# Kernel tuning notes

Hardware: AMD Instinct MI355X
Metric: run time of the kernel (lower is better)

## Reference

```python
import jax, jax.numpy as jnp
import numpy as np

K = 8

def setup_inputs() -> dict:
    key = jax.random.key(0)
    x = jax.random.normal(key, (64, 256, 56, 56), dtype=jnp.float32)
    return {"x": x}

def reference(x) -> jnp.ndarray:
    b, c, h, w = x.shape
    hw = h * w
    k = K if K < hw else hw - 1
    # topk indices computed on detached data (stop_gradient)
    data = jax.lax.stop_gradient(x).reshape(-1, hw)  # [b*c, hw]
    _, indices = jax.lax.top_k(data, k)              # [b*c, k]
    rows = jnp.arange(data.shape[0])[:, None]
    weight = jnp.zeros_like(data).at[rows, indices].set(1.0)
    # masked spatial sum -> [b, c]
    y = (x * weight.reshape(b, c, h, w)).sum(axis=(-1, -2))
    return y
```

## Files before the change

kernel.cpp:

```cpp
#include <hip/hip_runtime.h>


#define CE(a, b) { float _hi = fmaxf((a), (b)); float _lo = fminf((a), (b)); (a) = _hi; (b) = _lo; }

#define SORT4(s0, s1, s2, s3) { CE(s0, s2); CE(s1, s3); CE(s0, s1); CE(s2, s3); CE(s1, s2); }

#define MERGE4(l0, l1, l2, l3, l4, l5, l6, l7, s0, s1, s2, s3) { \
    l4 = fmaxf(l4, s3); l5 = fmaxf(l5, s2); l6 = fmaxf(l6, s1); l7 = fmaxf(l7, s0); \
    CE(l0, l4); CE(l1, l5); CE(l2, l6); CE(l3, l7); \
    CE(l0, l2); CE(l1, l3); CE(l4, l6); CE(l5, l7); \
    CE(l0, l1); CE(l2, l3); CE(l4, l5); CE(l6, l7); }

#define RESORT8(m0, m1, m2, m3, m4, m5, m6, m7) { \
    CE(m0, m4); CE(m1, m5); CE(m2, m6); CE(m3, m7); \
    CE(m0, m2); CE(m1, m3); CE(m4, m6); CE(m5, m7); \
    CE(m0, m1); CE(m2, m3); CE(m4, m5); CE(m6, m7); }

__global__ __launch_bounds__(256) void topk8_sum_kernel(
    const float* __restrict__ x, float* __restrict__ out, int rows) {
    const int gw = (int)((blockIdx.x * blockDim.x + threadIdx.x) >> 6);
    const int lane = (int)(threadIdx.x & 63);
    if (gw >= rows) return;

    const float* __restrict__ row = x + (size_t)gw * 3136;

    float a0 = -INFINITY, a1 = -INFINITY, a2 = -INFINITY, a3 = -INFINITY,
          a4 = -INFINITY, a5 = -INFINITY, a6 = -INFINITY, a7 = -INFINITY;
    float b0 = -INFINITY, b1 = -INFINITY, b2 = -INFINITY, b3 = -INFINITY,
          b4 = -INFINITY, b5 = -INFINITY, b6 = -INFINITY, b7 = -INFINITY;

    #pragma unroll
    for (int it = 0; it < 6; ++it) {
        float4 u = *reinterpret_cast<const float4*>(row + (2 * it) * 256 + lane * 4);
        float4 v = *reinterpret_cast<const float4*>(row + (2 * it + 1) * 256 + lane * 4);
        float u0 = u.x, u1 = u.y, u2 = u.z, u3 = u.w;
        float v0 = v.x, v1 = v.y, v2 = v.z, v3 = v.w;
        SORT4(u0, u1, u2, u3);
        SORT4(v0, v1, v2, v3);
        MERGE4(a0, a1, a2, a3, a4, a5, a6, a7, u0, u1, u2, u3);
        MERGE4(b0, b1, b2, b3, b4, b5, b6, b7, v0, v1, v2, v3);
    }

    {
        float t = row[3072 + lane];
        CE(b0, t); CE(b1, t); CE(b2, t); CE(b3, t);
        CE(b4, t); CE(b5, t); CE(b6, t); CE(b7, t);
    }

    float r0 = fmaxf(a0, b7), r1 = fmaxf(a1, b6), r2 = fmaxf(a2, b5), r3 = fmaxf(a3, b4),
          r4 = fmaxf(a4, b3), r5 = fmaxf(a5, b2), r6 = fmaxf(a6, b1), r7 = fmaxf(a7, b0);
    RESORT8(r0, r1, r2, r3, r4, r5, r6, r7);

    #pragma unroll
    for (int m = 1; m <= 16; m <<= 1) {
        float c0 = __shfl_xor(r0, m, 64);
        float c1 = __shfl_xor(r1, m, 64);
        float c2 = __shfl_xor(r2, m, 64);
        float c3 = __shfl_xor(r3, m, 64);
        float c4 = __shfl_xor(r4, m, 64);
        float c5 = __shfl_xor(r5, m, 64);
        float c6 = __shfl_xor(r6, m, 64);
        float c7 = __shfl_xor(r7, m, 64);
        float m0 = fmaxf(r0, c7), m1 = fmaxf(r1, c6), m2 = fmaxf(r2, c5), m3 = fmaxf(r3, c4),
              m4 = fmaxf(r4, c3), m5 = fmaxf(r5, c2), m6 = fmaxf(r6, c1), m7 = fmaxf(r7, c0);
        RESORT8(m0, m1, m2, m3, m4, m5, m6, m7);
        r0 = m0; r1 = m1; r2 = m2; r3 = m3;
        r4 = m4; r5 = m5; r6 = m6; r7 = m7;
    }

    {
        float c0 = __shfl_xor(r0, 32, 64);
        float c1 = __shfl_xor(r1, 32, 64);
        float c2 = __shfl_xor(r2, 32, 64);
        float c3 = __shfl_xor(r3, 32, 64);
        float c4 = __shfl_xor(r4, 32, 64);
        float c5 = __shfl_xor(r5, 32, 64);
        float c6 = __shfl_xor(r6, 32, 64);
        float c7 = __shfl_xor(r7, 32, 64);
        float sum = fmaxf(r0, c7) + fmaxf(r1, c6) + fmaxf(r2, c5) + fmaxf(r3, c4)
                  + fmaxf(r4, c3) + fmaxf(r5, c2) + fmaxf(r6, c1) + fmaxf(r7, c0);
        if (lane == 0) out[gw] = sum;
    }
}

extern "C" void kernel_launch(void* const* d_in, const int* in_sizes, int n_in,
                              void* d_out, int out_size, void* d_ws, size_t ws_size,
                              hipStream_t stream) {
    const float* x = (const float*)d_in[0];
    float* out = (float*)d_out;
    const int rows = out_size;
    const int threads = 256;
    const int blocks = (rows * 64 + threads - 1) / threads;
    topk8_sum_kernel<<<blocks, threads, 0, stream>>>(x, out, rows);
}
```

Baseline: 276.6 us.

## Make kernel persistent with register double-buffered row prefetch

Launches a fixed grid of 1024 blocks, each wave looping over rows with a grid stride. While processing the current row, it prefetches the next row's 49 floats per lane into registers, to overlap memory latency with the sorting network. This roughly doubles register use for row data, which may lower occupancy. It also cuts the number of resident waves compared with one wave per row.

New measurement: 277.9 us. About the same (+0.5%).

```diff
diff --git a/kernel.cpp b/kernel.cpp
--- a/kernel.cpp
+++ b/kernel.cpp
@@ -16,70 +16,92 @@
     CE(m0, m2); CE(m1, m3); CE(m4, m6); CE(m5, m7); \
     CE(m0, m1); CE(m2, m3); CE(m4, m5); CE(m6, m7); }
 
+struct RowData {
+    float4 q[12];
+    float t;
+};
+
+__device__ __forceinline__ RowData load_row(const float* __restrict__ p, int lane) {
+    RowData r;
+    #pragma unroll
+    for (int i = 0; i < 12; ++i)
+        r.q[i] = *reinterpret_cast<const float4*>(p + i * 256 + lane * 4);
+    r.t = p[3072 + lane];
+    return r;
+}
+
 __global__ __launch_bounds__(256) void topk8_sum_kernel(
-    const float* __restrict__ x, float* __restrict__ out, int rows) {
+    const float* __restrict__ x, float* __restrict__ out, int rows, int total_waves) {
     const int gw = (int)((blockIdx.x * blockDim.x + threadIdx.x) >> 6);
     const int lane = (int)(threadIdx.x & 63);
     if (gw >= rows) return;
 
-    const float* __restrict__ row = x + (size_t)gw * 3136;
+    RowData cur = load_row(x + (size_t)gw * 3136, lane);
 
-    float a0 = -INFINITY, a1 = -INFINITY, a2 = -INFINITY, a3 = -INFINITY,
-          a4 = -INFINITY, a5 = -INFINITY, a6 = -INFINITY, a7 = -INFINITY;
-    float b0 = -INFINITY, b1 = -INFINITY, b2 = -INFINITY, b3 = -INFINITY,
-          b4 = -INFINITY, b5 = -INFINITY, b6 = -INFINITY, b7 = -INFINITY;
+    for (int r = gw; r < rows; r += total_waves) {
+        const int next_r = r + total_waves;
+        RowData nxt;
+        if (next_r < rows)
+            nxt = load_row(x + (size_t)next_r * 3136, lane);
 
-    #pragma unroll
-    for (int it = 0; it < 6; ++it) {
-        float4 u = *reinterpret_cast<const float4*>(row + (2 * it) * 256 + lane * 4);
-        float4 v = *reinterpret_cast<const float4*>(row + (2 * it + 1) * 256 + lane * 4);
-        float u0 = u.x, u1 = u.y, u2 = u.z, u3 = u.w;
-        float v0 = v.x, v1 = v.y, v2 = v.z, v3 = v.w;
-        SORT4(u0, u1, u2, u3);
-        SORT4(v0, v1, v2, v3);
-        MERGE4(a0, a1, a2, a3, a4, a5, a6, a7, u0, u1, u2, u3);
-        MERGE4(b0, b1, b2, b3, b4, b5, b6, b7, v0, v1, v2, v3);
-    }
+        float a0 = -INFINITY, a1 = -INFINITY, a2 = -INFINITY, a3 = -INFINITY,
+              a4 = -INFINITY, a5 = -INFINITY, a6 = -INFINITY, a7 = -INFINITY;
+        float b0 = -INFINITY, b1 = -INFINITY, b2 = -INFINITY, b3 = -INFINITY,
+              b4 = -INFINITY, b5 = -INFINITY, b6 = -INFINITY, b7 = -INFINITY;
 
-    {
-        float t = row[3072 + lane];
-        CE(b0, t); CE(b1, t); CE(b2, t); CE(b3, t);
-        CE(b4, t); CE(b5, t); CE(b6, t); CE(b7, t);
-    }
+        #pragma unroll
+        for (int it = 0; it < 6; ++it) {
+            float4 u = cur.q[2 * it];
+            float4 v = cur.q[2 * it + 1];
+            float u0 = u.x, u1 = u.y, u2 = u.z, u3 = u.w;
+            float v0 = v.x, v1 = v.y, v2 = v.z, v3 = v.w;
+            SORT4(u0, u1, u2, u3);
+            SORT4(v0, v1, v2, v3);
+            MERGE4(a0, a1, a2, a3, a4, a5, a6, a7, u0, u1, u2, u3);
+            MERGE4(b0, b1, b2, b3, b4, b5, b6, b7, v0, v1, v2, v3);
+        }
+        {
+            float t = cur.t;
+            CE(b0, t); CE(b1, t); CE(b2, t); CE(b3, t);
+            CE(b4, t); CE(b5, t); CE(b6, t); CE(b7, t);
+        }
 
-    float r0 = fmaxf(a0, b7), r1 = fmaxf(a1, b6), r2 = fmaxf(a2, b5), r3 = fmaxf(a3, b4),
-          r4 = fmaxf(a4, b3), r5 = fmaxf(a5, b2), r6 = fmaxf(a6, b1), r7 = fmaxf(a7, b0);
-    RESORT8(r0, r1, r2, r3, r4, r5, r6, r7);
+        float r0 = fmaxf(a0, b7), r1 = fmaxf(a1, b6), r2 = fmaxf(a2, b5), r3 = fmaxf(a3, b4),
+              r4 = fmaxf(a4, b3), r5 = fmaxf(a5, b2), r6 = fmaxf(a6, b1), r7 = fmaxf(a7, b0);
+        RESORT8(r0, r1, r2, r3, r4, r5, r6, r7);
 
-    #pragma unroll
-    for (int m = 1; m <= 16; m <<= 1) {
-        float c0 = __shfl_xor(r0, m, 64);
-        float c1 = __shfl_xor(r1, m, 64);
-        float c2 = __shfl_xor(r2, m, 64);
-        float c3 = __shfl_xor(r3, m, 64);
-        float c4 = __shfl_xor(r4, m, 64);
-        float c5 = __shfl_xor(r5, m, 64);
-        float c6 = __shfl_xor(r6, m, 64);
-        float c7 = __shfl_xor(r7, m, 64);
-        float m0 = fmaxf(r0, c7), m1 = fmaxf(r1, c6), m2 = fmaxf(r2, c5), m3 = fmaxf(r3, c4),
-              m4 = fmaxf(r4, c3), m5 = fmaxf(r5, c2), m6 = fmaxf(r6, c1), m7 = fmaxf(r7, c0);
-        RESORT8(m0, m1, m2, m3, m4, m5, m6, m7);
-        r0 = m0; r1 = m1; r2 = m2; r3 = m3;
-        r4 = m4; r5 = m5; r6 = m6; r7 = m7;
-    }
+        #pragma unroll
+        for (int m = 1; m <= 16; m <<= 1) {
+            float c0 = __shfl_xor(r0, m, 64);
+            float c1 = __shfl_xor(r1, m, 64);
+            float c2 = __shfl_xor(r2, m, 64);
+            float c3 = __shfl_xor(r3, m, 64);
+            float c4 = __shfl_xor(r4, m, 64);
+            float c5 = __shfl_xor(r5, m, 64);
+            float c6 = __shfl_xor(r6, m, 64);
+            float c7 = __shfl_xor(r7, m, 64);
+            float m0 = fmaxf(r0, c7), m1 = fmaxf(r1, c6), m2 = fmaxf(r2, c5), m3 = fmaxf(r3, c4),
+                  m4 = fmaxf(r4, c3), m5 = fmaxf(r5, c2), m6 = fmaxf(r6, c1), m7 = fmaxf(r7, c0);
+            RESORT8(m0, m1, m2, m3, m4, m5, m6, m7);
+            r0 = m0; r1 = m1; r2 = m2; r3 = m3;
+            r4 = m4; r5 = m5; r6 = m6; r7 = m7;
+        }
 
-    {
-        float c0 = __shfl_xor(r0, 32, 64);
-        float c1 = __shfl_xor(r1, 32, 64);
-        float c2 = __shfl_xor(r2, 32, 64);
-        float c3 = __shfl_xor(r3, 32, 64);
-        float c4 = __shfl_xor(r4, 32, 64);
-        float c5 = __shfl_xor(r5, 32, 64);
-        float c6 = __shfl_xor(r6, 32, 64);
-        float c7 = __shfl_xor(r7, 32, 64);
-        float sum = fmaxf(r0, c7) + fmaxf(r1, c6) + fmaxf(r2, c5) + fmaxf(r3, c4)
-                  + fmaxf(r4, c3) + fmaxf(r5, c2) + fmaxf(r6, c1) + fmaxf(r7, c0);
-        if (lane == 0) out[gw] = sum;
+        {
+            float c0 = __shfl_xor(r0, 32, 64);
+            float c1 = __shfl_xor(r1, 32, 64);
+            float c2 = __shfl_xor(r2, 32, 64);
+            float c3 = __shfl_xor(r3, 32, 64);
+            float c4 = __shfl_xor(r4, 32, 64);
+            float c5 = __shfl_xor(r5, 32, 64);
+            float c6 = __shfl_xor(r6, 32, 64);
+            float c7 = __shfl_xor(r7, 32, 64);
+            float sum = fmaxf(r0, c7) + fmaxf(r1, c6) + fmaxf(r2, c5) + fmaxf(r3, c4)
+                      + fmaxf(r4, c3) + fmaxf(r5, c2) + fmaxf(r6, c1) + fmaxf(r7, c0);
+            if (lane == 0) out[r] = sum;
+        }
+
+        cur = nxt;
     }
 }
 
@@ -90,6 +112,7 @@
     float* out = (float*)d_out;
     const int rows = out_size;
     const int threads = 256;
-    const int blocks = (rows * 64 + threads - 1) / threads;
-    topk8_sum_kernel<<<blocks, threads, 0, stream>>>(x, out, rows);
+    const int blocks = 1024;
+    const int total_waves = blocks * (threads / 64);
+    topk8_sum_kernel<<<blocks, threads, 0, stream>>>(x, out, rows, total_waves);
 }
```
